# Kernel optimization log

Measured on AMD Instinct MI355X. Metric: run time of the kernel, lower is better.

The kernel has to match this reference:

```python
import jax, jax.numpy as jnp
import numpy as np

R = 2
K = 2 * R + 1  # kernel size 5


def _patches(x, axis):
    """Zero-padded sliding-window patches along `axis` for a [B,H,W,1] tensor.
    Mimics tf.image.extract_patches with SAME padding (zeros). Returns [B,H,W,K]."""
    pad = [(0, 0)] * 4
    pad[axis] = (R, R)
    xp = jnp.pad(x, pad)
    n = x.shape[axis]
    slices = [jax.lax.slice_in_dim(xp, i, i + n, axis=axis) for i in range(K)]
    return jnp.concatenate(slices, axis=-1)  # channel dim is 1 -> stacks taps


def _do_blur(bright_p, dark_p, depths_p, depths, spatial_dist, depth_var, spatial_var):
    # depth-guided weight, per tap
    rel = jnp.minimum(jnp.abs(depths_p / depths - 1.0), 1.0)
    w = jnp.exp(-jnp.square(rel) / (2.0 * depth_var)) * \
        jnp.exp(-jnp.square(spatial_dist) / (2.0 * spatial_var))
    w = w / jnp.sum(w, axis=-1, keepdims=True)
    b = jnp.sum(bright_p * w, axis=-1, keepdims=True)
    d = jnp.sum(dark_p * w, axis=-1, keepdims=True)
    return b, d


def _custom_pow(a, b):
    return jnp.exp(b * jnp.log(jnp.maximum(a, 1e-8)))


def setup_inputs() -> dict:
    key = jax.random.key(0)
    k1, k2, k3 = jax.random.split(key, 3)
    B, H, W = 8, 1024, 1024
    bright = jax.random.uniform(k1, (B, H, W, 1), dtype=jnp.float32)
    dark = jax.random.uniform(k2, (B, H, W, 1), dtype=jnp.float32)
    # depths are divided by; keep strictly positive
    depths = 0.1 + 0.9 * jax.random.uniform(k3, (B, H, W, 1), dtype=jnp.float32)
    return {
        "bright": bright,
        "dark": dark,
        "depths": depths,
        "depth_variance": jnp.float32(0.0004),
        "spatial_variance": jnp.float32(13.16),
        "dev_exponent": jnp.float32(0.3),
        "dark_epsilon": jnp.float32(0.375),
        "contrast_enhance": jnp.float32(0.95),
    }


def reference(bright, dark, depths, depth_variance, spatial_variance,
              dev_exponent, dark_epsilon, contrast_enhance):
    spatial_dist = jnp.arange(-R, R + 1, dtype=jnp.float32).reshape(1, 1, 1, K)
    # horizontal pass (along W = axis 2)
    bx, dx, zx = _patches(bright, 2), _patches(dark, 2), _patches(depths, 2)
    bright_x, dark_x = _do_blur(bx, dx, zx, depths, spatial_dist,
                                depth_variance, spatial_variance)
    # vertical pass (along H = axis 1) on horizontally-blurred values
    by, dy, zy = _patches(bright_x, 1), _patches(dark_x, 1), _patches(depths, 1)
    bright_mean, dark_mean = _do_blur(by, dy, zy, depths, spatial_dist,
                                      depth_variance, spatial_variance)
    # contrast-aware blend of bright/dark channels
    dev_bright = _custom_pow(jnp.abs(bright - bright_mean), dev_exponent)
    dev_dark = _custom_pow(jnp.abs(dark - dark_mean), dev_exponent)
    dev_dark = jnp.maximum(dev_dark, dark_epsilon)
    dev_bright = dev_bright * contrast_enhance
    wsum = dev_bright + dev_dark
    dev_bright = dev_bright / wsum
    dev_dark = dev_dark / wsum
    return dev_dark * bright + dev_bright * dark
```

## Files before the change

kernel.cpp:

```cpp
#include <hip/hip_runtime.h>

#define TH 8
#define W_ 1024
#define H_ 1024

__device__ __forceinline__ float wexp1(float zp, float iz, float kd, float kspat) {
    const float u = fmaf(zp, iz, -1.0f);
    return __builtin_amdgcn_exp2f(fmaf(u * kd, u, kspat));
}

__device__ __forceinline__ void blur5(
    float zm2, float zm1, float zc, float zp1, float zp2,
    float bm2, float bm1, float bc, float bp1, float bp2,
    float dm2, float dm1, float dc, float dp1, float dp2,
    float kd, float ks1, float ks4,
    float& ob, float& od)
{
    const float iz = __builtin_amdgcn_rcpf(zc);
    const float w0 = wexp1(zm2, iz, kd, ks4);
    const float w1 = wexp1(zm1, iz, kd, ks1);
    const float w3 = wexp1(zp1, iz, kd, ks1);
    const float w4 = wexp1(zp2, iz, kd, ks4);
    const float wr = __builtin_amdgcn_rcpf(1.0f + w0 + w1 + w3 + w4);
    ob = fmaf(w0, bm2, fmaf(w1, bm1, fmaf(w3, bp1, fmaf(w4, bp2, bc)))) * wr;
    od = fmaf(w0, dm2, fmaf(w1, dm1, fmaf(w3, dp1, fmaf(w4, dp2, dc)))) * wr;
}

__device__ __forceinline__ float blend1(float bc, float dc, float bm, float dm,
                                        float de, float dke, float ce) {
    const float devb = __builtin_amdgcn_exp2f(
        de * __builtin_amdgcn_logf(fmaxf(fabsf(bc - bm), 1e-8f))) * ce;
    const float devd = fmaxf(__builtin_amdgcn_exp2f(
        de * __builtin_amdgcn_logf(fmaxf(fabsf(dc - dm), 1e-8f))), dke);
    const float wr = __builtin_amdgcn_rcpf(devb + devd);
    return fmaf(devd, bc, devb * dc) * wr;
}

struct Raw {
    float2 lb, rb, ld, rd, lz, rz;
    float4 cb, cd, cz;
};

__device__ __forceinline__ void load_raw(
    int gy, const float* __restrict__ bB, const float* __restrict__ dB,
    const float* __restrict__ zB, int c, int colL2, int colR2, Raw& r)
{
    if ((unsigned)gy < (unsigned)H_) {
        const size_t ro = (size_t)gy * W_;
        r.lz = *(const float2*)(zB + ro + colL2);
        r.cz = *(const float4*)(zB + ro + c);
        r.rz = *(const float2*)(zB + ro + colR2);
        r.lb = *(const float2*)(bB + ro + colL2);
        r.cb = *(const float4*)(bB + ro + c);
        r.rb = *(const float2*)(bB + ro + colR2);
        r.ld = *(const float2*)(dB + ro + colL2);
        r.cd = *(const float4*)(dB + ro + c);
        r.rd = *(const float2*)(dB + ro + colR2);
    }
}

__device__ __forceinline__ void hblur_raw(
    int gy, const Raw& r, bool eL, bool eR,
    float kd, float ks1, float ks4,
    float4& sb, float4& sd, float4& sz)
{
    if ((unsigned)gy < (unsigned)H_) {
        float2 lz = r.lz, rz = r.rz;
        if (eL) { lz.x = 1e18f; lz.y = 1e18f; }
        if (eR) { rz.x = 1e18f; rz.y = 1e18f; }
        blur5(lz.x, lz.y, r.cz.x, r.cz.y, r.cz.z,
              r.lb.x, r.lb.y, r.cb.x, r.cb.y, r.cb.z,
              r.ld.x, r.ld.y, r.cd.x, r.cd.y, r.cd.z,
              kd, ks1, ks4, sb.x, sd.x);
        blur5(lz.y, r.cz.x, r.cz.y, r.cz.z, r.cz.w,
              r.lb.y, r.cb.x, r.cb.y, r.cb.z, r.cb.w,
              r.ld.y, r.cd.x, r.cd.y, r.cd.z, r.cd.w,
              kd, ks1, ks4, sb.y, sd.y);
        blur5(r.cz.x, r.cz.y, r.cz.z, r.cz.w, rz.x,
              r.cb.x, r.cb.y, r.cb.z, r.cb.w, r.rb.x,
              r.cd.x, r.cd.y, r.cd.z, r.cd.w, r.rd.x,
              kd, ks1, ks4, sb.z, sd.z);
        blur5(r.cz.y, r.cz.z, r.cz.w, rz.x, rz.y,
              r.cb.y, r.cb.z, r.cb.w, r.rb.x, r.rb.y,
              r.cd.y, r.cd.z, r.cd.w, r.rd.x, r.rd.y,
              kd, ks1, ks4, sb.w, sd.w);
        sz = r.cz;
    } else {
        sb = make_float4(0.f, 0.f, 0.f, 0.f);
        sd = make_float4(0.f, 0.f, 0.f, 0.f);
        sz = make_float4(0.f, 0.f, 0.f, 0.f);
    }
}

#define WSTEP(S, I)                                                           \
  {                                                                           \
    hblur_raw(y0 + (I) - 2, R, eL, eR, kd, ks1, ks4, pb[S], pd[S], pz[S]);    \
    load_raw(y0 + (I) - 1, bB, dB, zB, c, colL2, colR2, R);                   \
  }

#define FSTEP(S, S0, S1, S2, S3, S4, I, PREF)                                 \
  {                                                                           \
    hblur_raw(y0 + (I) - 2, R, eL, eR, kd, ks1, ks4, pb[S], pd[S], pz[S]);    \
    if (PREF) load_raw(y0 + (I) - 1, bB, dB, zB, c, colL2, colR2, R);         \
    const size_t oo = (size_t)(y0 + (I) - 4) * W_ + c;                        \
    const float4 rb4 = *(const float4*)(bB + oo);                             \
    const float4 rd4 = *(const float4*)(dB + oo);                             \
    float4 bm, dm;                                                            \
    blur5(pz[S0].x, pz[S1].x, pz[S2].x, pz[S3].x, pz[S4].x,                   \
          pb[S0].x, pb[S1].x, pb[S2].x, pb[S3].x, pb[S4].x,                   \
          pd[S0].x, pd[S1].x, pd[S2].x, pd[S3].x, pd[S4].x,                   \
          kd, ks1, ks4, bm.x, dm.x);                                          \
    blur5(pz[S0].y, pz[S1].y, pz[S2].y, pz[S3].y, pz[S4].y,                   \
          pb[S0].y, pb[S1].y, pb[S2].y, pb[S3].y, pb[S4].y,                   \
          pd[S0].y, pd[S1].y, pd[S2].y, pd[S3].y, pd[S4].y,                   \
          kd, ks1, ks4, bm.y, dm.y);                                          \
    blur5(pz[S0].z, pz[S1].z, pz[S2].z, pz[S3].z, pz[S4].z,                   \
          pb[S0].z, pb[S1].z, pb[S2].z, pb[S3].z, pb[S4].z,                   \
          pd[S0].z, pd[S1].z, pd[S2].z, pd[S3].z, pd[S4].z,                   \
          kd, ks1, ks4, bm.z, dm.z);                                          \
    blur5(pz[S0].w, pz[S1].w, pz[S2].w, pz[S3].w, pz[S4].w,                   \
          pb[S0].w, pb[S1].w, pb[S2].w, pb[S3].w, pb[S4].w,                   \
          pd[S0].w, pd[S1].w, pd[S2].w, pd[S3].w, pd[S4].w,                   \
          kd, ks1, ks4, bm.w, dm.w);                                          \
    float4 res;                                                               \
    res.x = blend1(rb4.x, rd4.x, bm.x, dm.x, de, dke, ce);                    \
    res.y = blend1(rb4.y, rd4.y, bm.y, dm.y, de, dke, ce);                    \
    res.z = blend1(rb4.z, rd4.z, bm.z, dm.z, de, dke, ce);                    \
    res.w = blend1(rb4.w, rd4.w, bm.w, dm.w, de, dke, ce);                    \
    *(float4*)(outB + oo) = res;                                              \
  }

__global__ __launch_bounds__(256, 4)
void bilateral_fused(const float* __restrict__ bright,
                     const float* __restrict__ dark,
                     const float* __restrict__ depths,
                     const float* __restrict__ p_dv,
                     const float* __restrict__ p_sv,
                     const float* __restrict__ p_de,
                     const float* __restrict__ p_deps,
                     const float* __restrict__ p_ce,
                     float* __restrict__ out)
{
    const float LOG2E = 1.44269504088896340736f;
    const float kd  = -LOG2E / (2.0f * p_dv[0]);
    const float ks  = -LOG2E / (2.0f * p_sv[0]);
    const float de  = p_de[0];
    const float dke = p_deps[0];
    const float ce  = p_ce[0];
    const float ks1 = ks;
    const float ks4 = 4.0f * ks;

    const int t  = threadIdx.x;
    const int c  = 4 * t;
    const int y0 = blockIdx.y * TH;

    const size_t plane = (size_t)H_ * W_;
    const float* bB = bright + (size_t)blockIdx.z * plane;
    const float* dB = dark   + (size_t)blockIdx.z * plane;
    const float* zB = depths + (size_t)blockIdx.z * plane;
    float*     outB = out    + (size_t)blockIdx.z * plane;

    const int  colL2 = max(c - 2, 0);
    const int  colR2 = min(c + 4, W_ - 2);
    const bool eL = (c == 0);
    const bool eR = (c + 4 >= W_);

    float4 pb[5], pd[5], pz[5];
    Raw R;

    load_raw(y0 - 2, bB, dB, zB, c, colL2, colR2, R);

    WSTEP(0, 0)
    WSTEP(1, 1)
    WSTEP(2, 2)
    WSTEP(3, 3)

    FSTEP(4, 0, 1, 2, 3, 4,  4, 1)
    FSTEP(0, 1, 2, 3, 4, 0,  5, 1)
    FSTEP(1, 2, 3, 4, 0, 1,  6, 1)
    FSTEP(2, 3, 4, 0, 1, 2,  7, 1)
    FSTEP(3, 4, 0, 1, 2, 3,  8, 1)
    FSTEP(4, 0, 1, 2, 3, 4,  9, 1)
    FSTEP(0, 1, 2, 3, 4, 0, 10, 1)
    FSTEP(1, 2, 3, 4, 0, 1, 11, 0)
}

extern "C" void kernel_launch(void* const* d_in, const int* in_sizes, int n_in,
                              void* d_out, int out_size, void* d_ws, size_t ws_size,
                              hipStream_t stream)
{
    const float* bright = (const float*)d_in[0];
    const float* dark   = (const float*)d_in[1];
    const float* depths = (const float*)d_in[2];
    const float* p_dv   = (const float*)d_in[3];
    const float* p_sv   = (const float*)d_in[4];
    const float* p_de   = (const float*)d_in[5];
    const float* p_deps = (const float*)d_in[6];
    const float* p_ce   = (const float*)d_in[7];
    float* out = (float*)d_out;

    const int B = in_sizes[0] / (H_ * W_);

    dim3 grid(1, H_ / TH, B);
    dim3 block(256);
    bilateral_fused<<<grid, block, 0, stream>>>(bright, dark, depths,
                                                p_dv, p_sv, p_de, p_deps, p_ce,
                                                out);
}
```

Before: 155.5 us.

## Replace software row prefetch with clamped loads, asm pins, and swizzled row-tile order

Removes the explicit one-row-ahead register prefetch. Each step now loads its row unconditionally with a clamped row index, and empty inline-asm uses pin the loaded values so all loads of a step issue together before the compute. Block row indices are also permuted (bit swizzle of blockIdx.y) so that concurrently running blocks touch rows spread across the image, which changes cache and DRAM access locality. Losing the cross-step prefetch may expose load latency, and the order swizzle could hurt L2 reuse of halo rows between adjacent tiles.

```diff
diff --git a/kernel.cpp b/kernel.cpp
--- a/kernel.cpp
+++ b/kernel.cpp
@@ -36,31 +36,42 @@
     return fmaf(devd, bc, devb * dc) * wr;
 }
 
-struct Raw {
-    float2 lb, rb, ld, rd, lz, rz;
-    float4 cb, cd, cz;
-};
-
-__device__ __forceinline__ void load_raw(
+struct Raw9 { float2 lz, rz, lb, rb, ld, rd; float4 cz, cb, cd; };
+
+__device__ __forceinline__ void load_row9(
     int gy, const float* __restrict__ bB, const float* __restrict__ dB,
-    const float* __restrict__ zB, int c, int colL2, int colR2, Raw& r)
-{
-    if ((unsigned)gy < (unsigned)H_) {
-        const size_t ro = (size_t)gy * W_;
-        r.lz = *(const float2*)(zB + ro + colL2);
-        r.cz = *(const float4*)(zB + ro + c);
-        r.rz = *(const float2*)(zB + ro + colR2);
-        r.lb = *(const float2*)(bB + ro + colL2);
-        r.cb = *(const float4*)(bB + ro + c);
-        r.rb = *(const float2*)(bB + ro + colR2);
-        r.ld = *(const float2*)(dB + ro + colL2);
-        r.cd = *(const float4*)(dB + ro + c);
-        r.rd = *(const float2*)(dB + ro + colR2);
-    }
-}
-
-__device__ __forceinline__ void hblur_raw(
-    int gy, const Raw& r, bool eL, bool eR,
+    const float* __restrict__ zB, int c, int colL2, int colR2, Raw9& r)
+{
+    const int gyc = min(max(gy, 0), H_ - 1);
+    const size_t ro = (size_t)gyc * W_;
+    r.lz = *(const float2*)(zB + ro + colL2);
+    r.cz = *(const float4*)(zB + ro + c);
+    r.rz = *(const float2*)(zB + ro + colR2);
+    r.lb = *(const float2*)(bB + ro + colL2);
+    r.cb = *(const float4*)(bB + ro + c);
+    r.rb = *(const float2*)(bB + ro + colR2);
+    r.ld = *(const float2*)(dB + ro + colL2);
+    r.cd = *(const float4*)(dB + ro + c);
+    r.rd = *(const float2*)(dB + ro + colR2);
+}
+
+#define P2(v) "v"((v).x), "v"((v).y)
+#define P4(v) "v"((v).x), "v"((v).y), "v"((v).z), "v"((v).w)
+
+__device__ __forceinline__ void pin_raw(const Raw9& r) {
+    asm volatile("" :: P2(r.lz), P4(r.cz), P2(r.rz),
+                       P2(r.lb), P4(r.cb), P2(r.rb),
+                       P2(r.ld), P4(r.cd), P2(r.rd));
+}
+__device__ __forceinline__ void pin_raw_blend(const Raw9& r,
+                                              const float4& a, const float4& b) {
+    asm volatile("" :: P2(r.lz), P4(r.cz), P2(r.rz),
+                       P2(r.lb), P4(r.cb), P2(r.rb),
+                       P2(r.ld), P4(r.cd), P2(r.rd), P4(a), P4(b));
+}
+
+__device__ __forceinline__ void hblur9(
+    int gy, const Raw9& r, bool eL, bool eR,
     float kd, float ks1, float ks4,
     float4& sb, float4& sd, float4& sz)
 {
@@ -94,17 +105,21 @@
 
 #define WSTEP(S, I)                                                           \
   {                                                                           \
-    hblur_raw(y0 + (I) - 2, R, eL, eR, kd, ks1, ks4, pb[S], pd[S], pz[S]);    \
-    load_raw(y0 + (I) - 1, bB, dB, zB, c, colL2, colR2, R);                   \
+    Raw9 r;                                                                   \
+    load_row9(y0 + (I) - 2, bB, dB, zB, c, colL2, colR2, r);                  \
+    pin_raw(r);                                                               \
+    hblur9(y0 + (I) - 2, r, eL, eR, kd, ks1, ks4, pb[S], pd[S], pz[S]);       \
   }
 
-#define FSTEP(S, S0, S1, S2, S3, S4, I, PREF)                                 \
+#define STEP(S, S0, S1, S2, S3, S4, I)                                        \
   {                                                                           \
-    hblur_raw(y0 + (I) - 2, R, eL, eR, kd, ks1, ks4, pb[S], pd[S], pz[S]);    \
-    if (PREF) load_raw(y0 + (I) - 1, bB, dB, zB, c, colL2, colR2, R);         \
+    Raw9 r;                                                                   \
+    load_row9(y0 + (I) - 2, bB, dB, zB, c, colL2, colR2, r);                  \
     const size_t oo = (size_t)(y0 + (I) - 4) * W_ + c;                        \
     const float4 rb4 = *(const float4*)(bB + oo);                             \
     const float4 rd4 = *(const float4*)(dB + oo);                             \
+    pin_raw_blend(r, rb4, rd4);                                               \
+    hblur9(y0 + (I) - 2, r, eL, eR, kd, ks1, ks4, pb[S], pd[S], pz[S]);       \
     float4 bm, dm;                                                            \
     blur5(pz[S0].x, pz[S1].x, pz[S2].x, pz[S3].x, pz[S4].x,                   \
           pb[S0].x, pb[S1].x, pb[S2].x, pb[S3].x, pb[S4].x,                   \
@@ -152,7 +167,10 @@
 
     const int t  = threadIdx.x;
     const int c  = 4 * t;
-    const int y0 = blockIdx.y * TH;
+
+    const int yl = blockIdx.y;
+    const int yt = ((yl & 7) << 4) | (yl >> 3);
+    const int y0 = yt * TH;
 
     const size_t plane = (size_t)H_ * W_;
     const float* bB = bright + (size_t)blockIdx.z * plane;
@@ -166,23 +184,20 @@
     const bool eR = (c + 4 >= W_);
 
     float4 pb[5], pd[5], pz[5];
-    Raw R;
-
-    load_raw(y0 - 2, bB, dB, zB, c, colL2, colR2, R);
 
     WSTEP(0, 0)
     WSTEP(1, 1)
     WSTEP(2, 2)
     WSTEP(3, 3)
 
-    FSTEP(4, 0, 1, 2, 3, 4,  4, 1)
-    FSTEP(0, 1, 2, 3, 4, 0,  5, 1)
-    FSTEP(1, 2, 3, 4, 0, 1,  6, 1)
-    FSTEP(2, 3, 4, 0, 1, 2,  7, 1)
-    FSTEP(3, 4, 0, 1, 2, 3,  8, 1)
-    FSTEP(4, 0, 1, 2, 3, 4,  9, 1)
-    FSTEP(0, 1, 2, 3, 4, 0, 10, 1)
-    FSTEP(1, 2, 3, 4, 0, 1, 11, 0)
+    STEP(4, 0, 1, 2, 3, 4,  4)
+    STEP(0, 1, 2, 3, 4, 0,  5)
+    STEP(1, 2, 3, 4, 0, 1,  6)
+    STEP(2, 3, 4, 0, 1, 2,  7)
+    STEP(3, 4, 0, 1, 2, 3,  8)
+    STEP(4, 0, 1, 2, 3, 4,  9)
+    STEP(0, 1, 2, 3, 4, 0, 10)
+    STEP(1, 2, 3, 4, 0, 1, 11)
 }
 
 extern "C" void kernel_launch(void* const* d_in, const int* in_sizes, int n_in,
```

New measurement: 158.7 us. 2.0% more time.

## Double-buffer row loads with inline asm and explicit vmcnt waits; swizzle row-tile order

Applied to the files above, without the earlier changes.

Row prefetches now go through inline-asm global loads into two alternating register buffers. Explicit s_waitcnt vmcnt counts let the next row's loads and the blend operands stay in flight while the current row is blurred, rather than leaving the compiler to insert conservative waits. Row indices are clamped so every load is issued unconditionally, which keeps the wait counts fixed. The block-to-row-tile mapping is also permuted so that neighbouring blocks in launch order work on distant row tiles, which may change cache and channel locality. The costs are higher register pressure and fragile hand-counted waitcnt values.

```diff
diff --git a/kernel.cpp b/kernel.cpp
--- a/kernel.cpp
+++ b/kernel.cpp
@@ -1,8 +1,34 @@
 #include <hip/hip_runtime.h>
+#include <stdint.h>
 
 #define TH 8
 #define W_ 1024
 #define H_ 1024
+
+typedef float v2f __attribute__((ext_vector_type(2)));
+typedef float v4f __attribute__((ext_vector_type(4)));
+
+#define ALOAD2(dst, ptr)                                                      \
+    asm volatile("global_load_dwordx2 %0, %1, off"                            \
+                 : "=v"(dst)                                                  \
+                 : "v"((unsigned long long)(uintptr_t)(const void*)(ptr))     \
+                 : "memory")
+#define ALOAD4(dst, ptr)                                                      \
+    asm volatile("global_load_dwordx4 %0, %1, off"                           \
+                 : "=v"(dst)                                                  \
+                 : "v"((unsigned long long)(uintptr_t)(const void*)(ptr))     \
+                 : "memory")
+
+#define AWAIT_RAW(N, r)                                                       \
+    asm volatile("s_waitcnt vmcnt(" #N ")"                                    \
+                 : "+v"((r).lz), "+v"((r).cz), "+v"((r).rz),                  \
+                   "+v"((r).lb), "+v"((r).cb), "+v"((r).rb),                  \
+                   "+v"((r).ld), "+v"((r).cd), "+v"((r).rd)                   \
+                 :: "memory")
+#define AWAIT_BL(N, a, b)                                                     \
+    asm volatile("s_waitcnt vmcnt(" #N ")" : "+v"(a), "+v"(b) :: "memory")
+
+struct RawA { v2f lz, rz, lb, rb, ld, rd; v4f cz, cb, cd; };
 
 __device__ __forceinline__ float wexp1(float zp, float iz, float kd, float kspat) {
     const float u = fmaf(zp, iz, -1.0f);
@@ -36,36 +62,30 @@
     return fmaf(devd, bc, devb * dc) * wr;
 }
 
-struct Raw {
-    float2 lb, rb, ld, rd, lz, rz;
-    float4 cb, cd, cz;
-};
-
-__device__ __forceinline__ void load_raw(
+__device__ __forceinline__ void aload_row(
     int gy, const float* __restrict__ bB, const float* __restrict__ dB,
-    const float* __restrict__ zB, int c, int colL2, int colR2, Raw& r)
-{
-    if ((unsigned)gy < (unsigned)H_) {
-        const size_t ro = (size_t)gy * W_;
-        r.lz = *(const float2*)(zB + ro + colL2);
-        r.cz = *(const float4*)(zB + ro + c);
-        r.rz = *(const float2*)(zB + ro + colR2);
-        r.lb = *(const float2*)(bB + ro + colL2);
-        r.cb = *(const float4*)(bB + ro + c);
-        r.rb = *(const float2*)(bB + ro + colR2);
-        r.ld = *(const float2*)(dB + ro + colL2);
-        r.cd = *(const float4*)(dB + ro + c);
-        r.rd = *(const float2*)(dB + ro + colR2);
-    }
-}
-
-__device__ __forceinline__ void hblur_raw(
-    int gy, const Raw& r, bool eL, bool eR,
+    const float* __restrict__ zB, int c, int colL2, int colR2, RawA& r)
+{
+    const int gyc = min(max(gy, 0), H_ - 1);
+    const size_t ro = (size_t)gyc * W_;
+    ALOAD2(r.lz, zB + ro + colL2);
+    ALOAD4(r.cz, zB + ro + c);
+    ALOAD2(r.rz, zB + ro + colR2);
+    ALOAD2(r.lb, bB + ro + colL2);
+    ALOAD4(r.cb, bB + ro + c);
+    ALOAD2(r.rb, bB + ro + colR2);
+    ALOAD2(r.ld, dB + ro + colL2);
+    ALOAD4(r.cd, dB + ro + c);
+    ALOAD2(r.rd, dB + ro + colR2);
+}
+
+__device__ __forceinline__ void hblur9(
+    int gy, const RawA& r, bool eL, bool eR,
     float kd, float ks1, float ks4,
     float4& sb, float4& sd, float4& sz)
 {
     if ((unsigned)gy < (unsigned)H_) {
-        float2 lz = r.lz, rz = r.rz;
+        v2f lz = r.lz, rz = r.rz;
         if (eL) { lz.x = 1e18f; lz.y = 1e18f; }
         if (eR) { rz.x = 1e18f; rz.y = 1e18f; }
         blur5(lz.x, lz.y, r.cz.x, r.cz.y, r.cz.z,
@@ -84,7 +104,7 @@
               r.cb.y, r.cb.z, r.cb.w, r.rb.x, r.rb.y,
               r.cd.y, r.cd.z, r.cd.w, r.rd.x, r.rd.y,
               kd, ks1, ks4, sb.w, sd.w);
-        sz = r.cz;
+        sz = make_float4(r.cz.x, r.cz.y, r.cz.z, r.cz.w);
     } else {
         sb = make_float4(0.f, 0.f, 0.f, 0.f);
         sd = make_float4(0.f, 0.f, 0.f, 0.f);
@@ -92,19 +112,22 @@
     }
 }
 
-#define WSTEP(S, I)                                                           \
+#define WSTEP(S, RC, RN, I)                                                   \
   {                                                                           \
-    hblur_raw(y0 + (I) - 2, R, eL, eR, kd, ks1, ks4, pb[S], pd[S], pz[S]);    \
-    load_raw(y0 + (I) - 1, bB, dB, zB, c, colL2, colR2, R);                   \
+    aload_row(y0 + (I) - 1, bB, dB, zB, c, colL2, colR2, RN);                 \
+    AWAIT_RAW(9, RC);                                                         \
+    hblur9(y0 + (I) - 2, RC, eL, eR, kd, ks1, ks4, pb[S], pd[S], pz[S]);      \
   }
 
-#define FSTEP(S, S0, S1, S2, S3, S4, I, PREF)                                 \
+#define FSTEP(S, S0, S1, S2, S3, S4, RC, RN, I, DOLOAD, NRAW, NBL)            \
   {                                                                           \
-    hblur_raw(y0 + (I) - 2, R, eL, eR, kd, ks1, ks4, pb[S], pd[S], pz[S]);    \
-    if (PREF) load_raw(y0 + (I) - 1, bB, dB, zB, c, colL2, colR2, R);         \
     const size_t oo = (size_t)(y0 + (I) - 4) * W_ + c;                        \
-    const float4 rb4 = *(const float4*)(bB + oo);                             \
-    const float4 rd4 = *(const float4*)(dB + oo);                             \
+    v4f rbv, rdv;                                                             \
+    ALOAD4(rbv, bB + oo);                                                     \
+    ALOAD4(rdv, dB + oo);                                                     \
+    if (DOLOAD) aload_row(y0 + (I) - 1, bB, dB, zB, c, colL2, colR2, RN);     \
+    AWAIT_RAW(NRAW, RC);                                                      \
+    hblur9(y0 + (I) - 2, RC, eL, eR, kd, ks1, ks4, pb[S], pd[S], pz[S]);      \
     float4 bm, dm;                                                            \
     blur5(pz[S0].x, pz[S1].x, pz[S2].x, pz[S3].x, pz[S4].x,                   \
           pb[S0].x, pb[S1].x, pb[S2].x, pb[S3].x, pb[S4].x,                   \
@@ -122,11 +145,12 @@
           pb[S0].w, pb[S1].w, pb[S2].w, pb[S3].w, pb[S4].w,                   \
           pd[S0].w, pd[S1].w, pd[S2].w, pd[S3].w, pd[S4].w,                   \
           kd, ks1, ks4, bm.w, dm.w);                                          \
+    AWAIT_BL(NBL, rbv, rdv);                                                  \
     float4 res;                                                               \
-    res.x = blend1(rb4.x, rd4.x, bm.x, dm.x, de, dke, ce);                    \
-    res.y = blend1(rb4.y, rd4.y, bm.y, dm.y, de, dke, ce);                    \
-    res.z = blend1(rb4.z, rd4.z, bm.z, dm.z, de, dke, ce);                    \
-    res.w = blend1(rb4.w, rd4.w, bm.w, dm.w, de, dke, ce);                    \
+    res.x = blend1(rbv.x, rdv.x, bm.x, dm.x, de, dke, ce);                    \
+    res.y = blend1(rbv.y, rdv.y, bm.y, dm.y, de, dke, ce);                    \
+    res.z = blend1(rbv.z, rdv.z, bm.z, dm.z, de, dke, ce);                    \
+    res.w = blend1(rbv.w, rdv.w, bm.w, dm.w, de, dke, ce);                    \
     *(float4*)(outB + oo) = res;                                              \
   }
 
@@ -152,7 +176,10 @@
 
     const int t  = threadIdx.x;
     const int c  = 4 * t;
-    const int y0 = blockIdx.y * TH;
+
+    const int yl = blockIdx.y;
+    const int yt = ((yl & 7) << 4) | (yl >> 3);
+    const int y0 = yt * TH;
 
     const size_t plane = (size_t)H_ * W_;
     const float* bB = bright + (size_t)blockIdx.z * plane;
@@ -166,23 +193,23 @@
     const bool eR = (c + 4 >= W_);
 
     float4 pb[5], pd[5], pz[5];
-    Raw R;
-
-    load_raw(y0 - 2, bB, dB, zB, c, colL2, colR2, R);
-
-    WSTEP(0, 0)
-    WSTEP(1, 1)
-    WSTEP(2, 2)
-    WSTEP(3, 3)
-
-    FSTEP(4, 0, 1, 2, 3, 4,  4, 1)
-    FSTEP(0, 1, 2, 3, 4, 0,  5, 1)
-    FSTEP(1, 2, 3, 4, 0, 1,  6, 1)
-    FSTEP(2, 3, 4, 0, 1, 2,  7, 1)
-    FSTEP(3, 4, 0, 1, 2, 3,  8, 1)
-    FSTEP(4, 0, 1, 2, 3, 4,  9, 1)
-    FSTEP(0, 1, 2, 3, 4, 0, 10, 1)
-    FSTEP(1, 2, 3, 4, 0, 1, 11, 0)
+    RawA rA, rB;
+
+    aload_row(y0 - 2, bB, dB, zB, c, colL2, colR2, rA);
+
+    WSTEP(0, rA, rB, 0)
+    WSTEP(1, rB, rA, 1)
+    WSTEP(2, rA, rB, 2)
+    WSTEP(3, rB, rA, 3)
+
+    FSTEP(4, 0, 1, 2, 3, 4,  rA, rB,  4, 1, 11, 9)
+    FSTEP(0, 1, 2, 3, 4, 0,  rB, rA,  5, 1, 11, 9)
+    FSTEP(1, 2, 3, 4, 0, 1,  rA, rB,  6, 1, 11, 9)
+    FSTEP(2, 3, 4, 0, 1, 2,  rB, rA,  7, 1, 11, 9)
+    FSTEP(3, 4, 0, 1, 2, 3,  rA, rB,  8, 1, 11, 9)
+    FSTEP(4, 0, 1, 2, 3, 4,  rB, rA,  9, 1, 11, 9)
+    FSTEP(0, 1, 2, 3, 4, 0,  rA, rB, 10, 1, 11, 9)
+    FSTEP(1, 2, 3, 4, 0, 1,  rB, rA, 11, 0,  2, 0)
 }
 
 extern "C" void kernel_launch(void* const* d_in, const int* in_sizes, int n_in,
```

After: 161.6 us. 1.04x slower.
